# Optimization experiments

Hardware: AMD Instinct MI355X
Metric: run time of the kernel (lower is better)

## Reference

```python
import jax, jax.numpy as jnp
import numpy as np

TH_HIGH = 0.6
TH_LOW = 0.3
NEGPOS_RATIO = 3
VAR0, VAR1 = 0.1, 0.2
IMG_SIZE = 255.0


def point_form(a):
    # (cx,cy,w,h) -> (xmin,ymin,xmax,ymax)
    return jnp.concatenate([a[..., :2] - a[..., 2:] / 2,
                            a[..., :2] + a[..., 2:] / 2], axis=-1)


def jaccard(a, b):
    # a: [B,4] point form, b: [A,4] point form -> IoU [B,A]
    lt = jnp.maximum(a[:, None, :2], b[None, :, :2])
    rb = jnp.minimum(a[:, None, 2:], b[None, :, 2:])
    wh = jnp.clip(rb - lt, 0.0)
    inter = wh[..., 0] * wh[..., 1]
    area_a = ((a[:, 2] - a[:, 0]) * (a[:, 3] - a[:, 1]))[:, None]
    area_b = ((b[:, 2] - b[:, 0]) * (b[:, 3] - b[:, 1]))[None, :]
    return inter / (area_a + area_b - inter)


def encode(matched, priors):
    # matched: point form, priors: center-size form (standard SSD encode)
    g_cxcy = ((matched[..., :2] + matched[..., 2:]) / 2 - priors[..., :2]) / (VAR0 * priors[..., 2:])
    g_wh = jnp.log((matched[..., 2:] - matched[..., :2]) / priors[..., 2:]) / VAR1
    return jnp.concatenate([g_cxcy, g_wh], axis=-1)


def decode(loc, priors):
    # standard SSD decode -> point form boxes
    cxcy = priors[..., :2] + loc[..., :2] * VAR0 * priors[..., 2:]
    wh = priors[..., 2:] * jnp.exp(loc[..., 2:] * VAR1)
    mins = cxcy - wh / 2
    return jnp.concatenate([mins, mins + wh], axis=-1)


def smooth_l1(x):
    ax = jnp.abs(x)
    return jnp.where(ax < 1.0, 0.5 * x * x, ax - 0.5)


def setup_inputs() -> dict:
    key = jax.random.key(0)
    k1, k2, k3, k4 = jax.random.split(key, 4)
    B, G, S = 64, 128, 4
    A = G * G * S  # 65536 anchors
    c = (jnp.arange(G, dtype=jnp.float32) + 0.5) / G
    cxcy = jnp.stack(jnp.meshgrid(c, c, indexing='ij'), axis=-1).reshape(-1, 2)  # [G*G,2]
    scales = jnp.array([0.08, 0.12, 0.2, 0.3], dtype=jnp.float32)
    wh = jnp.stack([scales, scales], axis=-1)  # [S,2]
    anchors = jnp.concatenate([jnp.repeat(cxcy, S, axis=0), jnp.tile(wh, (G * G, 1))], axis=-1)  # [A,4] center-size
    # gt boxes: small jitter around a random anchor so positives exist
    idx = jax.random.randint(k1, (B,), 0, A)
    gt_cs = anchors[idx] * (1.0 + 0.03 * jax.random.normal(k2, (B, 4), dtype=jnp.float32))
    gt_boxes = point_form(gt_cs)  # [B,4] point form
    loc_pred = 0.5 * jax.random.normal(k3, (B, A, 4), dtype=jnp.float32)
    conf_pred = jax.random.normal(k4, (B, A, 2), dtype=jnp.float32)
    return {"loc_pred": loc_pred, "conf_pred": conf_pred, "gt_boxes": gt_boxes, "anchors": anchors}


def reference(loc_pred, conf_pred, gt_boxes, anchors):
    B, A, _ = loc_pred.shape
    pf_anchors = point_form(anchors)
    overlaps = jaccard(gt_boxes, pf_anchors)                      # [B,A]
    labels = (overlaps >= TH_HIGH).astype(jnp.int32) - \
             ((overlaps > TH_LOW) & (overlaps < TH_HIGH)).astype(jnp.int32)
    pos = labels == 1                                             # [B,A]
    neg0 = labels == 0
    N = pos.sum()
    Nf = jnp.maximum(N.astype(loc_pred.dtype), 1.0)

    loc_gt = encode(gt_boxes[:, None, :], anchors[None, :, :])    # [B,A,4]
    elem = smooth_l1(loc_pred - loc_gt)
    loss_loc = (elem * pos[..., None]).sum() / (Nf * 4.0)

    # --- hard negative mining ---
    logp = jax.nn.log_softmax(conf_pred, axis=-1)                 # [B,A,2]
    tgt = pos.astype(jnp.int32)
    nll = -jnp.take_along_axis(logp, tgt[..., None], axis=-1)[..., 0]  # [B,A]
    ce = jnp.where(neg0, nll, 0.0)
    loss_idx = jnp.argsort(-ce, axis=1)                           # descending
    idx_rank = jnp.argsort(loss_idx, axis=1)
    num_pos = pos.sum(axis=1, keepdims=True)
    num_neg = jnp.clip(NEGPOS_RATIO * num_pos, 10, A - 1)
    neg = idx_rank < num_neg                                      # [B,A]

    # --- weighted classification loss over picked pos+neg ---
    sel = pos | neg
    w = jnp.array([1.0 / 3.0, 1.0], dtype=conf_pred.dtype)
    wsel = jnp.where(sel, w[tgt], 0.0)
    loss_cls = (nll * wsel).sum() / wsel.sum()

    # --- accuracies on picked set ---
    pred_cls = jnp.argmax(conf_pred, axis=-1)
    pos_m = sel & (tgt == 1)
    neg_m = sel & (tgt == 0)
    pos_accuracy = ((pred_cls == 1) & pos_m).sum() / jnp.maximum(pos_m.sum(), 1)
    neg_accuracy = ((pred_cls == 0) & neg_m).sum() / jnp.maximum(neg_m.sum(), 1)

    # --- decoded diagnostics (masked means over positives) ---
    decoded = decode(loc_pred, anchors[None, :, :])               # [B,A,4] point form
    pos_err = jnp.linalg.norm((gt_boxes[:, None, :2] - decoded[..., :2]) * IMG_SIZE, axis=-1)
    position_error = (pos_err * pos).sum() / Nf
    size_diff = jnp.abs(gt_boxes[:, None, 2:] - decoded[..., 2:])  # [B,A,2]
    size_errors = (size_diff * pos[..., None]).sum(axis=(0, 1)) / Nf * IMG_SIZE

    return (loss_loc, loss_cls, pos_accuracy, neg_accuracy, position_error, size_errors, N)
```

## Files before the change

kernel.cpp:

```cpp
#include <hip/hip_runtime.h>
#include <math.h>


#define MAXB 64
#define NS 1024
#define NB1 256
#define NB2 4096
#define NB3 2048

struct Accum {
  int row_np[MAXB];
  int row_eq_taken[MAXB];
  float f_loc[NS], f_clsp[NS], f_perr[NS], f_se0[NS], f_se1[NS], f_clsn[NS];
  int i_pcor[NS], i_ncor[NS], i_ntot[NS];
};

__device__ __forceinline__ float iou_f(float4 g, float4 an) {
  float ax0 = an.x - an.z * 0.5f, ay0 = an.y - an.w * 0.5f;
  float ax1 = an.x + an.z * 0.5f, ay1 = an.y + an.w * 0.5f;
  float ltx = fmaxf(g.x, ax0), lty = fmaxf(g.y, ay0);
  float rbx = fminf(g.z, ax1), rby = fminf(g.w, ay1);
  float w = fmaxf(rbx - ltx, 0.f), h = fmaxf(rby - lty, 0.f);
  float inter = w * h;
  float area_g = (g.z - g.x) * (g.w - g.y);
  float area_a = (ax1 - ax0) * (ay1 - ay0);
  return inter / (area_g + area_a - inter);
}

__device__ __forceinline__ float sl1(float x) {
  float ax = fabsf(x);
  return ax < 1.f ? 0.5f * x * x : ax - 0.5f;
}

template <int NB>
__device__ uint2 pick_hist(const unsigned int* __restrict__ h, int kr_in,
                           unsigned int* s_wsum,
                           volatile unsigned int* s_bin,
                           volatile unsigned int* s_kr) {
  int tid = threadIdx.x, lane = tid & 63, wv = tid >> 6;
  constexpr int PER = NB / 256;
  unsigned int loc[PER];
  unsigned int my = 0;
#pragma unroll
  for (int i = 0; i < PER; ++i) {
    loc[i] = h[tid * PER + i];
    my += loc[i];
  }
  unsigned int v = my;
#pragma unroll
  for (int o = 1; o < 64; o <<= 1) {
    unsigned int tv = __shfl_down(v, o, 64);
    if (lane + o < 64) v += tv;
  }
  if (lane == 0) s_wsum[wv] = v;
  __syncthreads();
  unsigned int off = 0;
  for (int w2 = wv + 1; w2 < 4; ++w2) off += s_wsum[w2];
  unsigned int vw = v;
  unsigned int incl = vw + off;
  unsigned int above = incl - my;
  if ((int)above < kr_in && kr_in <= (int)incl) {
    int kk = kr_in - (int)above;
    for (int i = PER - 1; i >= 0; --i) {
      int c = (int)loc[i];
      if (kk <= c) {
        *s_bin = (unsigned int)(tid * PER + i);
        *s_kr = (unsigned int)kk;
        break;
      }
      kk -= c;
    }
  }
  __syncthreads();
  uint2 r;
  r.x = *s_bin;
  r.y = *s_kr;
  __syncthreads();
  return r;
}

__device__ __forceinline__ int row_k(const Accum* acc, int b, int A) {
  int k = 3 * acc->row_np[b];
  if (k < 10) k = 10;
  if (k > A - 1) k = A - 1;
  return k;
}

__global__ __launch_bounds__(256) void k_init(Accum* acc, unsigned int* g1,
                                              unsigned int* g2,
                                              unsigned int* g3) {
  int idx = blockIdx.x * 256 + threadIdx.x;
  int stride = gridDim.x * 256;
  int n0 = (int)(sizeof(Accum) / 4);
  int* p = (int*)acc;
  for (int i = idx; i < n0; i += stride) p[i] = 0;
  for (int i = idx; i < MAXB * NB1; i += stride) g1[i] = 0u;
  for (int i = idx; i < MAXB * NB2; i += stride) g2[i] = 0u;
  for (int i = idx; i < MAXB * NB3; i += stride) g3[i] = 0u;
}

__global__ __launch_bounds__(256) void k_main(
    const float* __restrict__ loc_pred, const float* __restrict__ conf,
    const float* __restrict__ gt, const float* __restrict__ anchors,
    Accum* __restrict__ acc, unsigned int* __restrict__ g1,
    unsigned int* __restrict__ keys, int A) {
  int b = blockIdx.y;
  int tid = threadIdx.x;
  int lane = tid & 63, wv = tid >> 6;
  __shared__ unsigned int hist[4][NB1];
  __shared__ float smf[5][4];
  __shared__ int smi[2][4];
  for (int i = tid; i < 4 * NB1; i += 256) ((unsigned int*)hist)[i] = 0u;
  __syncthreads();

  float4 g4 = reinterpret_cast<const float4*>(gt)[b];
  const float4* conf4 = reinterpret_cast<const float4*>(conf);
  const float4* anc4 = reinterpret_cast<const float4*>(anchors);
  const float4* loc4 = reinterpret_cast<const float4*>(loc_pred);
  int abase = blockIdx.x * 4096;
  long long cbase = ((long long)b * A + abase) >> 1;
  uint2* keys2 = reinterpret_cast<uint2*>(keys);

  float loc_s = 0.f, clsp = 0.f, perr = 0.f, se0 = 0.f, se1 = 0.f;
  int pcnt = 0, pcor = 0;

#pragma unroll
  for (int j = 0; j < 8; ++j) {
    float4 cc = conf4[cbase + tid + j * 256];
    int a0 = abase + 2 * (tid + j * 256);
    uint2 kv;
#pragma unroll
    for (int h = 0; h < 2; ++h) {
      int a = a0 + h;
      float c0 = h ? cc.z : cc.x;
      float c1 = h ? cc.w : cc.y;
      float4 an = anc4[a];
      float ov = iou_f(g4, an);
      unsigned int kk = 0u;
      if (ov <= 0.3f) {
        float m = fmaxf(c0, c1);
        float s = logf(expf(c0 - m) + expf(c1 - m));
        kk = __float_as_uint((m - c0) + s);
      }
      if (c1 > c0) kk |= 0x80000000u;
      if (h) kv.y = kk; else kv.x = kk;
      atomicAdd(&hist[wv][(kk & 0x7FFFFFFFu) >> 23], 1u);
      if (ov >= 0.6f) {
        float4 lp = loc4[(long long)b * A + a];
        float gcx = (g4.x + g4.z) * 0.5f, gcy = (g4.y + g4.w) * 0.5f;
        float gw = g4.z - g4.x, gh = g4.w - g4.y;
        float t0 = (gcx - an.x) / (0.1f * an.z);
        float t1 = (gcy - an.y) / (0.1f * an.w);
        float t2 = logf(gw / an.z) / 0.2f;
        float t3 = logf(gh / an.w) / 0.2f;
        loc_s += sl1(lp.x - t0) + sl1(lp.y - t1) + sl1(lp.z - t2) +
                 sl1(lp.w - t3);
        float m = fmaxf(c0, c1);
        float s = logf(expf(c0 - m) + expf(c1 - m));
        clsp += (m - c1) + s;
        pcnt += 1;
        pcor += (c1 > c0) ? 1 : 0;
        float dcx = an.x + lp.x * 0.1f * an.z;
        float dcy = an.y + lp.y * 0.1f * an.w;
        float dw = an.z * expf(lp.z * 0.2f);
        float dh = an.w * expf(lp.w * 0.2f);
        float dx0 = dcx - dw * 0.5f, dy0 = dcy - dh * 0.5f;
        float ex = (g4.x - dx0) * 255.f, ey = (g4.y - dy0) * 255.f;
        perr += sqrtf(ex * ex + ey * ey);
        se0 += fabsf(g4.z - (dx0 + dw));
        se1 += fabsf(g4.w - (dy0 + dh));
      }
    }
    keys2[cbase + tid + j * 256] = kv;
  }

  __syncthreads();
  for (int i = tid; i < NB1; i += 256) {
    unsigned int h = hist[0][i] + hist[1][i] + hist[2][i] + hist[3][i];
    if (h) atomicAdd(&g1[b * NB1 + i], h);
  }

  float fv[5] = {loc_s, clsp, perr, se0, se1};
  int iv[2] = {pcnt, pcor};
#pragma unroll
  for (int q = 0; q < 5; ++q) {
    float v = fv[q];
#pragma unroll
    for (int o = 32; o > 0; o >>= 1) v += __shfl_down(v, o, 64);
    if (lane == 0) smf[q][wv] = v;
  }
#pragma unroll
  for (int q = 0; q < 2; ++q) {
    int v = iv[q];
#pragma unroll
    for (int o = 32; o > 0; o >>= 1) v += __shfl_down(v, o, 64);
    if (lane == 0) smi[q][wv] = v;
  }
  __syncthreads();
  if (tid == 0) {
    float L = 0, C = 0, P = 0, S0 = 0, S1 = 0;
    int PC = 0, COR = 0;
    for (int w2 = 0; w2 < 4; ++w2) {
      L += smf[0][w2]; C += smf[1][w2]; P += smf[2][w2];
      S0 += smf[3][w2]; S1 += smf[4][w2];
      PC += smi[0][w2]; COR += smi[1][w2];
    }
    if (PC > 0) {
      int slot = (blockIdx.y * gridDim.x + blockIdx.x) & (NS - 1);
      atomicAdd(&acc->row_np[b], PC);
      atomicAdd(&acc->f_loc[slot], L);
      atomicAdd(&acc->f_clsp[slot], C);
      atomicAdd(&acc->f_perr[slot], P);
      atomicAdd(&acc->f_se0[slot], S0);
      atomicAdd(&acc->f_se1[slot], S1);
      atomicAdd(&acc->i_pcor[slot], COR);
    }
  }
}

__device__ __forceinline__ void load_keys16(const unsigned int* __restrict__ keys,
                                            int b, int A, unsigned int* kk) {
  long long base4 = (((long long)b * A) >> 2) + blockIdx.x * 1024 + threadIdx.x;
  const uint4* k4 = reinterpret_cast<const uint4*>(keys);
#pragma unroll
  for (int j = 0; j < 4; ++j) {
    uint4 v = k4[base4 + j * 256];
    kk[4 * j + 0] = v.x; kk[4 * j + 1] = v.y;
    kk[4 * j + 2] = v.z; kk[4 * j + 3] = v.w;
  }
}

__global__ __launch_bounds__(256) void k_h2(const unsigned int* __restrict__ keys,
                                            const unsigned int* __restrict__ g1,
                                            unsigned int* __restrict__ g2,
                                            Accum* __restrict__ acc, int A) {
  int b = blockIdx.y;
  __shared__ unsigned int s_wsum[4];
  __shared__ unsigned int s_bin, s_kr;
  uint2 p1 = pick_hist<NB1>(g1 + b * NB1, row_k(acc, b, A), s_wsum, &s_bin, &s_kr);
  unsigned int kk[16];
  load_keys16(keys, b, A, kk);
#pragma unroll
  for (int j = 0; j < 16; ++j) {
    unsigned int k31 = kk[j] & 0x7FFFFFFFu;
    if ((k31 >> 23) == p1.x)
      atomicAdd(&g2[b * NB2 + ((k31 >> 11) & 0xFFFu)], 1u);
  }
}

__global__ __launch_bounds__(256) void k_h3(const unsigned int* __restrict__ keys,
                                            const unsigned int* __restrict__ g1,
                                            const unsigned int* __restrict__ g2,
                                            unsigned int* __restrict__ g3,
                                            Accum* __restrict__ acc, int A) {
  int b = blockIdx.y;
  __shared__ unsigned int s_wsum[4];
  __shared__ unsigned int s_bin, s_kr;
  uint2 p1 = pick_hist<NB1>(g1 + b * NB1, row_k(acc, b, A), s_wsum, &s_bin, &s_kr);
  uint2 p2 = pick_hist<NB2>(g2 + b * NB2, (int)p1.y, s_wsum, &s_bin, &s_kr);
  unsigned int pref20 = (p1.x << 12) | p2.x;
  unsigned int kk[16];
  load_keys16(keys, b, A, kk);
#pragma unroll
  for (int j = 0; j < 16; ++j) {
    unsigned int k31 = kk[j] & 0x7FFFFFFFu;
    if ((k31 >> 11) == pref20) atomicAdd(&g3[b * NB3 + (k31 & 0x7FFu)], 1u);
  }
}

__global__ __launch_bounds__(256) void k_neg(const unsigned int* __restrict__ keys,
                                             const unsigned int* __restrict__ g1,
                                             const unsigned int* __restrict__ g2,
                                             const unsigned int* __restrict__ g3,
                                             Accum* __restrict__ acc, int A) {
  int b = blockIdx.y;
  int tid = threadIdx.x;
  int lane = tid & 63, wv = tid >> 6;
  __shared__ unsigned int s_wsum[4];
  __shared__ unsigned int s_bin, s_kr;
  __shared__ float smf[4];
  __shared__ int smi[2][4];
  uint2 p1 = pick_hist<NB1>(g1 + b * NB1, row_k(acc, b, A), s_wsum, &s_bin, &s_kr);
  uint2 p2 = pick_hist<NB2>(g2 + b * NB2, (int)p1.y, s_wsum, &s_bin, &s_kr);
  uint2 p3 = pick_hist<NB3>(g3 + b * NB3, (int)p2.y, s_wsum, &s_bin, &s_kr);
  unsigned int thr = (p1.x << 23) | (p2.x << 11) | p3.x;
  int need = (int)p3.y;

  unsigned int kk[16];
  load_keys16(keys, b, A, kk);
  float cls = 0.f;
  int ncnt = 0, ncor = 0;
#pragma unroll
  for (int j = 0; j < 16; ++j) {
    unsigned int k31 = kk[j] & 0x7FFFFFFFu;
    bool s = false;
    if (k31 > thr) {
      s = true;
    } else if (k31 == thr) {
      int ord = atomicAdd(&acc->row_eq_taken[b], 1);
      if (ord < need) s = true;
    }
    if (s) {
      cls += __uint_as_float(k31);
      ncnt += 1;
      ncor += (int)((kk[j] >> 31) ^ 1u);
    }
  }
  {
    float v = cls;
#pragma unroll
    for (int o = 32; o > 0; o >>= 1) v += __shfl_down(v, o, 64);
    if (lane == 0) smf[wv] = v;
  }
  {
    int v = ncnt;
#pragma unroll
    for (int o = 32; o > 0; o >>= 1) v += __shfl_down(v, o, 64);
    if (lane == 0) smi[0][wv] = v;
  }
  {
    int v = ncor;
#pragma unroll
    for (int o = 32; o > 0; o >>= 1) v += __shfl_down(v, o, 64);
    if (lane == 0) smi[1][wv] = v;
  }
  __syncthreads();
  if (tid == 0) {
    float C = smf[0] + smf[1] + smf[2] + smf[3];
    int NC = smi[0][0] + smi[0][1] + smi[0][2] + smi[0][3];
    int COR = smi[1][0] + smi[1][1] + smi[1][2] + smi[1][3];
    if (NC > 0) {
      int slot = (blockIdx.y * gridDim.x + blockIdx.x) & (NS - 1);
      atomicAdd(&acc->f_clsn[slot], C);
      atomicAdd(&acc->i_ntot[slot], NC);
      atomicAdd(&acc->i_ncor[slot], COR);
    }
  }
}

__global__ __launch_bounds__(256) void k_final(const Accum* __restrict__ acc,
                                               float* __restrict__ out, int B) {
  __shared__ float sm[256];
  int t = threadIdx.x;
  float vals[10];
  float s;
  s = 0; for (int i = t; i < NS; i += 256) s += acc->f_loc[i];  vals[0] = s;
  s = 0; for (int i = t; i < NS; i += 256) s += acc->f_clsp[i]; vals[1] = s;
  s = 0; for (int i = t; i < NS; i += 256) s += acc->f_perr[i]; vals[2] = s;
  s = 0; for (int i = t; i < NS; i += 256) s += acc->f_se0[i];  vals[3] = s;
  s = 0; for (int i = t; i < NS; i += 256) s += acc->f_se1[i];  vals[4] = s;
  s = 0; for (int i = t; i < NS; i += 256) s += acc->f_clsn[i]; vals[5] = s;
  s = 0; for (int i = t; i < NS; i += 256) s += (float)acc->i_pcor[i]; vals[6] = s;
  s = 0; for (int i = t; i < NS; i += 256) s += (float)acc->i_ncor[i]; vals[7] = s;
  s = 0; for (int i = t; i < NS; i += 256) s += (float)acc->i_ntot[i]; vals[8] = s;
  s = 0; for (int i = t; i < B;  i += 256) s += (float)acc->row_np[i]; vals[9] = s;
  float tot[10];
  for (int q = 0; q < 10; ++q) {
    sm[t] = vals[q];
    __syncthreads();
    for (int o = 128; o > 0; o >>= 1) {
      if (t < o) sm[t] += sm[t + o];
      __syncthreads();
    }
    tot[q] = sm[0];
    __syncthreads();
  }
  if (t == 0) {
    float N = tot[9];
    float Nf = fmaxf(N, 1.f);
    out[0] = tot[0] / (Nf * 4.f);
    float wsum = N + tot[8] * (1.f / 3.f);
    out[1] = (tot[1] + tot[5] * (1.f / 3.f)) / wsum;
    out[2] = tot[6] / fmaxf(N, 1.f);
    out[3] = tot[7] / fmaxf(tot[8], 1.f);
    out[4] = tot[2] / Nf;
    out[5] = tot[3] / Nf * 255.f;
    out[6] = tot[4] / Nf * 255.f;
    out[7] = N;
  }
}

extern "C" void kernel_launch(void* const* d_in, const int* in_sizes, int n_in,
                              void* d_out, int out_size, void* d_ws,
                              size_t ws_size, hipStream_t stream) {
  (void)n_in; (void)out_size; (void)ws_size;
  const float* loc = (const float*)d_in[0];
  const float* conf = (const float*)d_in[1];
  const float* gt = (const float*)d_in[2];
  const float* anchors = (const float*)d_in[3];
  int B = in_sizes[2] / 4;
  int A = in_sizes[3] / 4;
  float* out = (float*)d_out;

  char* w = (char*)d_ws;
  Accum* acc = (Accum*)w;
  size_t off = (sizeof(Accum) + 255) & ~(size_t)255;
  unsigned int* g1 = (unsigned int*)(w + off);
  off += (size_t)MAXB * NB1 * 4;
  unsigned int* g2 = (unsigned int*)(w + off);
  off += (size_t)MAXB * NB2 * 4;
  unsigned int* g3 = (unsigned int*)(w + off);
  off += (size_t)MAXB * NB3 * 4;
  off = (off + 255) & ~(size_t)255;
  unsigned int* keys = (unsigned int*)(w + off);

  dim3 grid(A / 4096, B);
  k_init<<<128, 256, 0, stream>>>(acc, g1, g2, g3);
  k_main<<<grid, 256, 0, stream>>>(loc, conf, gt, anchors, acc, g1, keys, A);
  k_h2<<<grid, 256, 0, stream>>>(keys, g1, g2, acc, A);
  k_h3<<<grid, 256, 0, stream>>>(keys, g1, g2, g3, acc, A);
  k_neg<<<grid, 256, 0, stream>>>(keys, g1, g2, g3, acc, A);
  k_final<<<1, 256, 0, stream>>>(acc, out, B);
}
```

Measured before the change: 174.4 us.

## Fuse radix-select passes into one per-row block kernel with last-block finalize

Replaces the init, three global-histogram radix passes, and final reduction kernels with a single per-row 1024-thread kernel. Each block keeps all 65536 keys of its row in registers and runs the three-level radix select in shared memory. The last block to finish then does the final reduction. Per-block partial sums are written to slots instead of accumulated atomically, which removes the zero-init kernel. This cuts launches, global atomics and repeated key reads, but runs only 64 blocks for the select phase and uses 64 key registers per thread, so occupancy drops.

```diff
diff --git a/kernel.cpp b/kernel.cpp
--- a/kernel.cpp
+++ b/kernel.cpp
@@ -3,16 +3,13 @@
 
 
 #define MAXB 64
-#define NS 1024
-#define NB1 256
-#define NB2 4096
-#define NB3 2048
+#define NSLOT 1024
 
 struct Accum {
-  int row_np[MAXB];
-  int row_eq_taken[MAXB];
-  float f_loc[NS], f_clsp[NS], f_perr[NS], f_se0[NS], f_se1[NS], f_clsn[NS];
-  int i_pcor[NS], i_ncor[NS], i_ntot[NS];
+  float f_loc[NSLOT], f_clsp[NSLOT], f_perr[NSLOT], f_se0[NSLOT], f_se1[NSLOT];
+  int i_pcor[NSLOT], i_pcnt[NSLOT];
+  float f_clsn;
+  unsigned int i_ncor, i_ntot, done;
 };
 
 __device__ __forceinline__ float iou_f(float4 g, float4 an) {
@@ -32,86 +29,15 @@
   return ax < 1.f ? 0.5f * x * x : ax - 0.5f;
 }
 
-template <int NB>
-__device__ uint2 pick_hist(const unsigned int* __restrict__ h, int kr_in,
-                           unsigned int* s_wsum,
-                           volatile unsigned int* s_bin,
-                           volatile unsigned int* s_kr) {
-  int tid = threadIdx.x, lane = tid & 63, wv = tid >> 6;
-  constexpr int PER = NB / 256;
-  unsigned int loc[PER];
-  unsigned int my = 0;
-#pragma unroll
-  for (int i = 0; i < PER; ++i) {
-    loc[i] = h[tid * PER + i];
-    my += loc[i];
-  }
-  unsigned int v = my;
-#pragma unroll
-  for (int o = 1; o < 64; o <<= 1) {
-    unsigned int tv = __shfl_down(v, o, 64);
-    if (lane + o < 64) v += tv;
-  }
-  if (lane == 0) s_wsum[wv] = v;
-  __syncthreads();
-  unsigned int off = 0;
-  for (int w2 = wv + 1; w2 < 4; ++w2) off += s_wsum[w2];
-  unsigned int vw = v;
-  unsigned int incl = vw + off;
-  unsigned int above = incl - my;
-  if ((int)above < kr_in && kr_in <= (int)incl) {
-    int kk = kr_in - (int)above;
-    for (int i = PER - 1; i >= 0; --i) {
-      int c = (int)loc[i];
-      if (kk <= c) {
-        *s_bin = (unsigned int)(tid * PER + i);
-        *s_kr = (unsigned int)kk;
-        break;
-      }
-      kk -= c;
-    }
-  }
-  __syncthreads();
-  uint2 r;
-  r.x = *s_bin;
-  r.y = *s_kr;
-  __syncthreads();
-  return r;
-}
-
-__device__ __forceinline__ int row_k(const Accum* acc, int b, int A) {
-  int k = 3 * acc->row_np[b];
-  if (k < 10) k = 10;
-  if (k > A - 1) k = A - 1;
-  return k;
-}
-
-__global__ __launch_bounds__(256) void k_init(Accum* acc, unsigned int* g1,
-                                              unsigned int* g2,
-                                              unsigned int* g3) {
-  int idx = blockIdx.x * 256 + threadIdx.x;
-  int stride = gridDim.x * 256;
-  int n0 = (int)(sizeof(Accum) / 4);
-  int* p = (int*)acc;
-  for (int i = idx; i < n0; i += stride) p[i] = 0;
-  for (int i = idx; i < MAXB * NB1; i += stride) g1[i] = 0u;
-  for (int i = idx; i < MAXB * NB2; i += stride) g2[i] = 0u;
-  for (int i = idx; i < MAXB * NB3; i += stride) g3[i] = 0u;
-}
-
 __global__ __launch_bounds__(256) void k_main(
     const float* __restrict__ loc_pred, const float* __restrict__ conf,
     const float* __restrict__ gt, const float* __restrict__ anchors,
-    Accum* __restrict__ acc, unsigned int* __restrict__ g1,
-    unsigned int* __restrict__ keys, int A) {
+    Accum* __restrict__ acc, unsigned int* __restrict__ keys, int A) {
   int b = blockIdx.y;
   int tid = threadIdx.x;
   int lane = tid & 63, wv = tid >> 6;
-  __shared__ unsigned int hist[4][NB1];
   __shared__ float smf[5][4];
   __shared__ int smi[2][4];
-  for (int i = tid; i < 4 * NB1; i += 256) ((unsigned int*)hist)[i] = 0u;
-  __syncthreads();
 
   float4 g4 = reinterpret_cast<const float4*>(gt)[b];
   const float4* conf4 = reinterpret_cast<const float4*>(conf);
@@ -144,7 +70,6 @@
       }
       if (c1 > c0) kk |= 0x80000000u;
       if (h) kv.y = kk; else kv.x = kk;
-      atomicAdd(&hist[wv][(kk & 0x7FFFFFFFu) >> 23], 1u);
       if (ov >= 0.6f) {
         float4 lp = loc4[(long long)b * A + a];
         float gcx = (g4.x + g4.z) * 0.5f, gcy = (g4.y + g4.w) * 0.5f;
@@ -174,12 +99,6 @@
     keys2[cbase + tid + j * 256] = kv;
   }
 
-  __syncthreads();
-  for (int i = tid; i < NB1; i += 256) {
-    unsigned int h = hist[0][i] + hist[1][i] + hist[2][i] + hist[3][i];
-    if (h) atomicAdd(&g1[b * NB1 + i], h);
-  }
-
   float fv[5] = {loc_s, clsp, perr, se0, se1};
   int iv[2] = {pcnt, pcor};
 #pragma unroll
@@ -205,100 +124,159 @@
       S0 += smf[3][w2]; S1 += smf[4][w2];
       PC += smi[0][w2]; COR += smi[1][w2];
     }
-    if (PC > 0) {
-      int slot = (blockIdx.y * gridDim.x + blockIdx.x) & (NS - 1);
-      atomicAdd(&acc->row_np[b], PC);
-      atomicAdd(&acc->f_loc[slot], L);
-      atomicAdd(&acc->f_clsp[slot], C);
-      atomicAdd(&acc->f_perr[slot], P);
-      atomicAdd(&acc->f_se0[slot], S0);
-      atomicAdd(&acc->f_se1[slot], S1);
-      atomicAdd(&acc->i_pcor[slot], COR);
-    }
-  }
-}
-
-__device__ __forceinline__ void load_keys16(const unsigned int* __restrict__ keys,
-                                            int b, int A, unsigned int* kk) {
-  long long base4 = (((long long)b * A) >> 2) + blockIdx.x * 1024 + threadIdx.x;
+    int slot = b * gridDim.x + blockIdx.x;
+    acc->f_loc[slot] = L;
+    acc->f_clsp[slot] = C;
+    acc->f_perr[slot] = P;
+    acc->f_se0[slot] = S0;
+    acc->f_se1[slot] = S1;
+    acc->i_pcor[slot] = COR;
+    acc->i_pcnt[slot] = PC;
+    if (slot == 0) {
+      acc->f_clsn = 0.f;
+      acc->i_ncor = 0u;
+      acc->i_ntot = 0u;
+      acc->done = 0u;
+    }
+  }
+}
+
+template <int NB>
+__device__ __forceinline__ uint2 pick1024(const unsigned int* cnt, int kr_in,
+                                          unsigned int* s_wsum,
+                                          unsigned int* s_bin,
+                                          unsigned int* s_kr) {
+  const int tid = threadIdx.x, lane = tid & 63, wv = tid >> 6;
+  constexpr int PER = NB / 1024;
+  unsigned int my = 0;
+#pragma unroll
+  for (int i = 0; i < PER; ++i) my += cnt[i];
+  unsigned int v = my;
+#pragma unroll
+  for (int o = 1; o < 64; o <<= 1) {
+    unsigned int tv = __shfl_down(v, o, 64);
+    if (lane + o < 64) v += tv;
+  }
+  if (lane == 0) s_wsum[wv] = v;
+  __syncthreads();
+  unsigned int off = 0;
+#pragma unroll
+  for (int w2 = 0; w2 < 16; ++w2)
+    if (w2 > wv) off += s_wsum[w2];
+  unsigned int incl = v + off;
+  unsigned int above = incl - my;
+  if ((int)above < kr_in && kr_in <= (int)incl) {
+    int kk = kr_in - (int)above;
+#pragma unroll
+    for (int i = PER - 1; i >= 0; --i) {
+      int c = (int)cnt[i];
+      if (kk <= c) {
+        *s_bin = (unsigned int)(tid * PER + i);
+        *s_kr = (unsigned int)kk;
+        break;
+      }
+      kk -= c;
+    }
+  }
+  __syncthreads();
+  uint2 r;
+  r.x = *s_bin;
+  r.y = *s_kr;
+  __syncthreads();
+  return r;
+}
+
+__global__ __launch_bounds__(1024) void k_select(
+    const unsigned int* __restrict__ keys, Accum* __restrict__ acc,
+    float* __restrict__ out, int A, int spr) {
+  int b = blockIdx.x;
+  int tid = threadIdx.x;
+  int lane = tid & 63, wv = tid >> 6;
+  __shared__ unsigned int h1[4][2048];
+  __shared__ unsigned int h2[1024];
+  __shared__ unsigned int h3[1024];
+  __shared__ unsigned int s_wsum[16];
+  __shared__ unsigned int s_bin, s_kr;
+  __shared__ int s_npar[16];
+  __shared__ unsigned int s_eq;
+  __shared__ unsigned int s_lastf;
+  __shared__ float s_nf[16];
+  __shared__ int s_ni[2][16];
+  __shared__ float s_rf[5][16];
+  __shared__ int s_ri[2][16];
+
+  unsigned int* hz = &h1[0][0];
+#pragma unroll
+  for (int i = 0; i < 8; ++i) hz[tid + i * 1024] = 0u;
+  h2[tid] = 0u;
+  h3[tid] = 0u;
+  if (tid < spr) s_npar[tid] = acc->i_pcnt[b * spr + tid];
+  if (tid == 0) s_eq = 0u;
+
+  unsigned int kk[64];
   const uint4* k4 = reinterpret_cast<const uint4*>(keys);
-#pragma unroll
-  for (int j = 0; j < 4; ++j) {
-    uint4 v = k4[base4 + j * 256];
+  long long base4 = ((long long)b * A) >> 2;
+#pragma unroll
+  for (int j = 0; j < 16; ++j) {
+    uint4 v = k4[base4 + tid + j * 1024];
     kk[4 * j + 0] = v.x; kk[4 * j + 1] = v.y;
     kk[4 * j + 2] = v.z; kk[4 * j + 3] = v.w;
   }
-}
-
-__global__ __launch_bounds__(256) void k_h2(const unsigned int* __restrict__ keys,
-                                            const unsigned int* __restrict__ g1,
-                                            unsigned int* __restrict__ g2,
-                                            Accum* __restrict__ acc, int A) {
-  int b = blockIdx.y;
-  __shared__ unsigned int s_wsum[4];
-  __shared__ unsigned int s_bin, s_kr;
-  uint2 p1 = pick_hist<NB1>(g1 + b * NB1, row_k(acc, b, A), s_wsum, &s_bin, &s_kr);
-  unsigned int kk[16];
-  load_keys16(keys, b, A, kk);
-#pragma unroll
-  for (int j = 0; j < 16; ++j) {
+  __syncthreads();
+
+  int np = 0;
+#pragma unroll
+  for (int i = 0; i < 16; ++i) np += (i < spr) ? s_npar[i] : 0;
+  int k = 3 * np;
+  if (k < 10) k = 10;
+  if (k > A - 1) k = A - 1;
+
+  unsigned int* hw = h1[wv >> 2];
+#pragma unroll
+  for (int j = 0; j < 64; ++j)
+    atomicAdd(&hw[(kk[j] & 0x7FFFFFFFu) >> 20], 1u);
+  __syncthreads();
+  unsigned int c1l[2];
+#pragma unroll
+  for (int i = 0; i < 2; ++i) {
+    int bin = 2 * tid + i;
+    c1l[i] = h1[0][bin] + h1[1][bin] + h1[2][bin] + h1[3][bin];
+  }
+  uint2 p1 = pick1024<2048>(c1l, k, s_wsum, &s_bin, &s_kr);
+
+#pragma unroll
+  for (int j = 0; j < 64; ++j) {
     unsigned int k31 = kk[j] & 0x7FFFFFFFu;
-    if ((k31 >> 23) == p1.x)
-      atomicAdd(&g2[b * NB2 + ((k31 >> 11) & 0xFFFu)], 1u);
-  }
-}
-
-__global__ __launch_bounds__(256) void k_h3(const unsigned int* __restrict__ keys,
-                                            const unsigned int* __restrict__ g1,
-                                            const unsigned int* __restrict__ g2,
-                                            unsigned int* __restrict__ g3,
-                                            Accum* __restrict__ acc, int A) {
-  int b = blockIdx.y;
-  __shared__ unsigned int s_wsum[4];
-  __shared__ unsigned int s_bin, s_kr;
-  uint2 p1 = pick_hist<NB1>(g1 + b * NB1, row_k(acc, b, A), s_wsum, &s_bin, &s_kr);
-  uint2 p2 = pick_hist<NB2>(g2 + b * NB2, (int)p1.y, s_wsum, &s_bin, &s_kr);
-  unsigned int pref20 = (p1.x << 12) | p2.x;
-  unsigned int kk[16];
-  load_keys16(keys, b, A, kk);
-#pragma unroll
-  for (int j = 0; j < 16; ++j) {
+    if ((k31 >> 20) == p1.x) atomicAdd(&h2[(k31 >> 10) & 0x3FFu], 1u);
+  }
+  __syncthreads();
+  unsigned int c2l = h2[tid];
+  uint2 p2 = pick1024<1024>(&c2l, (int)p1.y, s_wsum, &s_bin, &s_kr);
+
+  unsigned int pref21 = (p1.x << 10) | p2.x;
+#pragma unroll
+  for (int j = 0; j < 64; ++j) {
     unsigned int k31 = kk[j] & 0x7FFFFFFFu;
-    if ((k31 >> 11) == pref20) atomicAdd(&g3[b * NB3 + (k31 & 0x7FFu)], 1u);
-  }
-}
-
-__global__ __launch_bounds__(256) void k_neg(const unsigned int* __restrict__ keys,
-                                             const unsigned int* __restrict__ g1,
-                                             const unsigned int* __restrict__ g2,
-                                             const unsigned int* __restrict__ g3,
-                                             Accum* __restrict__ acc, int A) {
-  int b = blockIdx.y;
-  int tid = threadIdx.x;
-  int lane = tid & 63, wv = tid >> 6;
-  __shared__ unsigned int s_wsum[4];
-  __shared__ unsigned int s_bin, s_kr;
-  __shared__ float smf[4];
-  __shared__ int smi[2][4];
-  uint2 p1 = pick_hist<NB1>(g1 + b * NB1, row_k(acc, b, A), s_wsum, &s_bin, &s_kr);
-  uint2 p2 = pick_hist<NB2>(g2 + b * NB2, (int)p1.y, s_wsum, &s_bin, &s_kr);
-  uint2 p3 = pick_hist<NB3>(g3 + b * NB3, (int)p2.y, s_wsum, &s_bin, &s_kr);
-  unsigned int thr = (p1.x << 23) | (p2.x << 11) | p3.x;
+    if ((k31 >> 10) == pref21) atomicAdd(&h3[k31 & 0x3FFu], 1u);
+  }
+  __syncthreads();
+  unsigned int c3l = h3[tid];
+  uint2 p3 = pick1024<1024>(&c3l, (int)p2.y, s_wsum, &s_bin, &s_kr);
+
+  unsigned int thr = (pref21 << 10) | p3.x;
   int need = (int)p3.y;
 
-  unsigned int kk[16];
-  load_keys16(keys, b, A, kk);
   float cls = 0.f;
   int ncnt = 0, ncor = 0;
 #pragma unroll
-  for (int j = 0; j < 16; ++j) {
+  for (int j = 0; j < 64; ++j) {
     unsigned int k31 = kk[j] & 0x7FFFFFFFu;
     bool s = false;
     if (k31 > thr) {
       s = true;
     } else if (k31 == thr) {
-      int ord = atomicAdd(&acc->row_eq_taken[b], 1);
-      if (ord < need) s = true;
+      unsigned int ord = atomicAdd(&s_eq, 1u);
+      if ((int)ord < need) s = true;
     }
     if (s) {
       cls += __uint_as_float(k31);
@@ -310,73 +288,93 @@
     float v = cls;
 #pragma unroll
     for (int o = 32; o > 0; o >>= 1) v += __shfl_down(v, o, 64);
-    if (lane == 0) smf[wv] = v;
+    if (lane == 0) s_nf[wv] = v;
   }
   {
     int v = ncnt;
 #pragma unroll
     for (int o = 32; o > 0; o >>= 1) v += __shfl_down(v, o, 64);
-    if (lane == 0) smi[0][wv] = v;
+    if (lane == 0) s_ni[0][wv] = v;
   }
   {
     int v = ncor;
 #pragma unroll
     for (int o = 32; o > 0; o >>= 1) v += __shfl_down(v, o, 64);
-    if (lane == 0) smi[1][wv] = v;
+    if (lane == 0) s_ni[1][wv] = v;
   }
   __syncthreads();
   if (tid == 0) {
-    float C = smf[0] + smf[1] + smf[2] + smf[3];
-    int NC = smi[0][0] + smi[0][1] + smi[0][2] + smi[0][3];
-    int COR = smi[1][0] + smi[1][1] + smi[1][2] + smi[1][3];
-    if (NC > 0) {
-      int slot = (blockIdx.y * gridDim.x + blockIdx.x) & (NS - 1);
-      atomicAdd(&acc->f_clsn[slot], C);
-      atomicAdd(&acc->i_ntot[slot], NC);
-      atomicAdd(&acc->i_ncor[slot], COR);
-    }
-  }
-}
-
-__global__ __launch_bounds__(256) void k_final(const Accum* __restrict__ acc,
-                                               float* __restrict__ out, int B) {
-  __shared__ float sm[256];
-  int t = threadIdx.x;
-  float vals[10];
-  float s;
-  s = 0; for (int i = t; i < NS; i += 256) s += acc->f_loc[i];  vals[0] = s;
-  s = 0; for (int i = t; i < NS; i += 256) s += acc->f_clsp[i]; vals[1] = s;
-  s = 0; for (int i = t; i < NS; i += 256) s += acc->f_perr[i]; vals[2] = s;
-  s = 0; for (int i = t; i < NS; i += 256) s += acc->f_se0[i];  vals[3] = s;
-  s = 0; for (int i = t; i < NS; i += 256) s += acc->f_se1[i];  vals[4] = s;
-  s = 0; for (int i = t; i < NS; i += 256) s += acc->f_clsn[i]; vals[5] = s;
-  s = 0; for (int i = t; i < NS; i += 256) s += (float)acc->i_pcor[i]; vals[6] = s;
-  s = 0; for (int i = t; i < NS; i += 256) s += (float)acc->i_ncor[i]; vals[7] = s;
-  s = 0; for (int i = t; i < NS; i += 256) s += (float)acc->i_ntot[i]; vals[8] = s;
-  s = 0; for (int i = t; i < B;  i += 256) s += (float)acc->row_np[i]; vals[9] = s;
-  float tot[10];
-  for (int q = 0; q < 10; ++q) {
-    sm[t] = vals[q];
+    float C = 0;
+    int NC = 0, COR = 0;
+    for (int w2 = 0; w2 < 16; ++w2) {
+      C += s_nf[w2];
+      NC += s_ni[0][w2];
+      COR += s_ni[1][w2];
+    }
+    atomicAdd(&acc->f_clsn, C);
+    atomicAdd(&acc->i_ntot, (unsigned int)NC);
+    atomicAdd(&acc->i_ncor, (unsigned int)COR);
+  }
+
+  __threadfence();
+  if (tid == 0) {
+    unsigned int old = __hip_atomic_fetch_add(&acc->done, 1u, __ATOMIC_ACQ_REL,
+                                              __HIP_MEMORY_SCOPE_AGENT);
+    s_lastf = (old == (unsigned int)(gridDim.x - 1)) ? 1u : 0u;
+  }
+  __syncthreads();
+  if (s_lastf) {
+    __threadfence();
+    float fv[5];
+    int iv[2];
+    fv[0] = acc->f_loc[tid];
+    fv[1] = acc->f_clsp[tid];
+    fv[2] = acc->f_perr[tid];
+    fv[3] = acc->f_se0[tid];
+    fv[4] = acc->f_se1[tid];
+    iv[0] = acc->i_pcor[tid];
+    iv[1] = acc->i_pcnt[tid];
+#pragma unroll
+    for (int q = 0; q < 5; ++q) {
+      float v = fv[q];
+#pragma unroll
+      for (int o = 32; o > 0; o >>= 1) v += __shfl_down(v, o, 64);
+      if (lane == 0) s_rf[q][wv] = v;
+    }
+#pragma unroll
+    for (int q = 0; q < 2; ++q) {
+      int v = iv[q];
+#pragma unroll
+      for (int o = 32; o > 0; o >>= 1) v += __shfl_down(v, o, 64);
+      if (lane == 0) s_ri[q][wv] = v;
+    }
     __syncthreads();
-    for (int o = 128; o > 0; o >>= 1) {
-      if (t < o) sm[t] += sm[t + o];
-      __syncthreads();
-    }
-    tot[q] = sm[0];
-    __syncthreads();
-  }
-  if (t == 0) {
-    float N = tot[9];
-    float Nf = fmaxf(N, 1.f);
-    out[0] = tot[0] / (Nf * 4.f);
-    float wsum = N + tot[8] * (1.f / 3.f);
-    out[1] = (tot[1] + tot[5] * (1.f / 3.f)) / wsum;
-    out[2] = tot[6] / fmaxf(N, 1.f);
-    out[3] = tot[7] / fmaxf(tot[8], 1.f);
-    out[4] = tot[2] / Nf;
-    out[5] = tot[3] / Nf * 255.f;
-    out[6] = tot[4] / Nf * 255.f;
-    out[7] = N;
+    if (tid == 0) {
+      float T[5] = {0, 0, 0, 0, 0};
+      int TI[2] = {0, 0};
+      for (int w2 = 0; w2 < 16; ++w2) {
+        T[0] += s_rf[0][w2]; T[1] += s_rf[1][w2]; T[2] += s_rf[2][w2];
+        T[3] += s_rf[3][w2]; T[4] += s_rf[4][w2];
+        TI[0] += s_ri[0][w2]; TI[1] += s_ri[1][w2];
+      }
+      float clsn = __hip_atomic_load(&acc->f_clsn, __ATOMIC_RELAXED,
+                                     __HIP_MEMORY_SCOPE_AGENT);
+      unsigned int ntot = __hip_atomic_load(&acc->i_ntot, __ATOMIC_RELAXED,
+                                            __HIP_MEMORY_SCOPE_AGENT);
+      unsigned int ncr = __hip_atomic_load(&acc->i_ncor, __ATOMIC_RELAXED,
+                                           __HIP_MEMORY_SCOPE_AGENT);
+      float N = (float)TI[1];
+      float Nf = fmaxf(N, 1.f);
+      out[0] = T[0] / (Nf * 4.f);
+      float wsum = N + (float)ntot * (1.f / 3.f);
+      out[1] = (T[1] + clsn * (1.f / 3.f)) / wsum;
+      out[2] = (float)TI[0] / fmaxf(N, 1.f);
+      out[3] = (float)ncr / fmaxf((float)ntot, 1.f);
+      out[4] = T[2] / Nf;
+      out[5] = T[3] / Nf * 255.f;
+      out[6] = T[4] / Nf * 255.f;
+      out[7] = N;
+    }
   }
 }
 
@@ -395,20 +393,10 @@
   char* w = (char*)d_ws;
   Accum* acc = (Accum*)w;
   size_t off = (sizeof(Accum) + 255) & ~(size_t)255;
-  unsigned int* g1 = (unsigned int*)(w + off);
-  off += (size_t)MAXB * NB1 * 4;
-  unsigned int* g2 = (unsigned int*)(w + off);
-  off += (size_t)MAXB * NB2 * 4;
-  unsigned int* g3 = (unsigned int*)(w + off);
-  off += (size_t)MAXB * NB3 * 4;
-  off = (off + 255) & ~(size_t)255;
   unsigned int* keys = (unsigned int*)(w + off);
 
-  dim3 grid(A / 4096, B);
-  k_init<<<128, 256, 0, stream>>>(acc, g1, g2, g3);
-  k_main<<<grid, 256, 0, stream>>>(loc, conf, gt, anchors, acc, g1, keys, A);
-  k_h2<<<grid, 256, 0, stream>>>(keys, g1, g2, acc, A);
-  k_h3<<<grid, 256, 0, stream>>>(keys, g1, g2, g3, acc, A);
-  k_neg<<<grid, 256, 0, stream>>>(keys, g1, g2, g3, acc, A);
-  k_final<<<1, 256, 0, stream>>>(acc, out, B);
-}
+  int spr = A / 4096;
+  dim3 grid(spr, B);
+  k_main<<<grid, 256, 0, stream>>>(loc, conf, gt, anchors, acc, keys, A);
+  k_select<<<B, 1024, 0, stream>>>(keys, acc, out, A, spr);
+}
```

Result: slower. 187.0 us (+7.2%).
